# Kernel optimization log

Hardware: AMD Instinct MI355X
Metric: run time of the kernel (lower is better)

The kernel has to match this reference:

```python
import jax, jax.numpy as jnp
import numpy as np

DIM = 1024
NUM_HEADS = 16
HEAD_DIM = DIM // NUM_HEADS


def setup_inputs() -> dict:
    key = jax.random.key(0)
    k1, k2, k3, k4, k5 = jax.random.split(key, 5)
    B, N, C = 8, 1024, DIM
    x = jax.random.normal(k1, (B, N, C), dtype=jnp.float32)
    s_in = 1.0 / np.sqrt(C)
    w_qkv = jax.random.normal(k2, (C, 3 * C), dtype=jnp.float32) * s_in
    b_qkv = jnp.zeros((3 * C,), dtype=jnp.float32)
    w_proj = jax.random.normal(k3, (C, C), dtype=jnp.float32) * s_in
    b_proj = jnp.zeros((C,), dtype=jnp.float32)
    return {"x": x, "w_qkv": w_qkv, "b_qkv": b_qkv, "w_proj": w_proj, "b_proj": b_proj}


def reference(x, w_qkv, b_qkv, w_proj, b_proj):
    B, N, C = x.shape
    H, D = NUM_HEADS, C // NUM_HEADS
    scale = jnp.float32(1.0) / jnp.sqrt(jnp.float32(D))
    qkv = x @ w_qkv + b_qkv                      # [B, N, 3C]
    qkv = qkv.reshape(B, N, 3, H, D)
    qkv = jnp.transpose(qkv, (2, 0, 3, 1, 4))     # [3, B, H, N, D]
    q, k, v = qkv[0], qkv[1], qkv[2]
    attn = jnp.einsum('bhnd,bhmd->bhnm', q, k) * scale  # [B, H, N, N]
    attn = jax.nn.softmax(attn, axis=-1)
    out = jnp.einsum('bhnm,bhmd->bhnd', attn, v)  # [B, H, N, D]
    out = jnp.transpose(out, (0, 2, 1, 3)).reshape(B, N, C)
    return out @ w_proj + b_proj
```

## Files before the change

### kernel.cpp

```cpp
#include <hip/hip_runtime.h>
#include <stdint.h>
#include <stddef.h>


#define DEVI __device__ __forceinline__

typedef float f32x4 __attribute__((ext_vector_type(4)));
typedef float f32x16 __attribute__((ext_vector_type(16)));
typedef __bf16 bf16x8 __attribute__((ext_vector_type(8)));
typedef unsigned short u16x8 __attribute__((ext_vector_type(8)));
typedef unsigned short u16x4 __attribute__((ext_vector_type(4)));
typedef unsigned int u32;
typedef unsigned int u32x4 __attribute__((ext_vector_type(4)));

static constexpr int M1 = 8192;

DEVI unsigned short f2bf(float f) {
  uint32_t u = __builtin_bit_cast(uint32_t, f);
  u += 0x7FFFu + ((u >> 16) & 1u);
  return (unsigned short)(u >> 16);
}

DEVI float fexp2(float x) {
  float r;
  asm("v_exp_f32 %0, %1" : "=v"(r) : "v"(x));
  return r;
}

DEVI u32 cvtpk(float lo, float hi) {
  u32 r;
  asm("v_cvt_pk_bf16_f32 %0, %1, %2" : "=v"(r) : "v"(lo), "v"(hi));
  return r;
}

DEVI void plswap(u32& a, u32& b) {
  asm("v_permlane32_swap_b32 %0, %1" : "+v"(a), "+v"(b));
}

DEVI void gll16(const unsigned short* g, unsigned short* lds) {
  __builtin_amdgcn_global_load_lds(
      (const __attribute__((address_space(1))) void*)g,
      (__attribute__((address_space(3))) void*)lds, 16, 0, 0);
}

DEVI bf16x8 lds_frag(const unsigned short* p) {
  return __builtin_bit_cast(bf16x8, *(const u16x8*)p);
}

__global__ void k_cvt(const float* __restrict__ in, unsigned short* __restrict__ out, int n4) {
  int i = blockIdx.x * blockDim.x + threadIdx.x;
  if (i < n4) {
    float4 v = reinterpret_cast<const float4*>(in)[i];
    u16x4 o = { f2bf(v.x), f2bf(v.y), f2bf(v.z), f2bf(v.w) };
    reinterpret_cast<u16x4*>(out)[i] = o;
  }
}

__global__ void k_tr_cvt(const float* __restrict__ in, unsigned short* __restrict__ out,
                         int R, int Cc) {
  __shared__ float tile[32][33];
  int c0 = blockIdx.x * 32, r0 = blockIdx.y * 32;
  int tx = threadIdx.x, ty = threadIdx.y;
#pragma unroll
  for (int j = 0; j < 32; j += 8)
    tile[ty + j][tx] = in[(size_t)(r0 + ty + j) * Cc + c0 + tx];
  __syncthreads();
#pragma unroll
  for (int j = 0; j < 32; j += 8)
    out[(size_t)(c0 + ty + j) * R + r0 + tx] = f2bf(tile[tx][ty + j]);
}

__global__ void k_tr_v(const unsigned short* __restrict__ in, unsigned short* __restrict__ out) {
  __shared__ unsigned short t[32][33];
  int d0 = blockIdx.x * 32, n0 = blockIdx.y * 32, bh = blockIdx.z;
  const unsigned short* ip = in + (size_t)bh * 1024 * 64;
  unsigned short* op = out + (size_t)bh * 64 * 1024;
  int tx = threadIdx.x, ty = threadIdx.y;
#pragma unroll
  for (int j = 0; j < 32; j += 8)
    t[ty + j][tx] = ip[(size_t)(n0 + ty + j) * 64 + d0 + tx];
  __syncthreads();
#pragma unroll
  for (int j = 0; j < 32; j += 8)
    op[(size_t)(d0 + ty + j) * 1024 + n0 + tx] = t[tx][ty + j];
}

template <int EPI, int NCOLS>
__global__ __launch_bounds__(256, 2)
void k_gemm(const unsigned short* __restrict__ A,
            const unsigned short* __restrict__ Bt,
            const float* __restrict__ bias,
            unsigned short* __restrict__ Qp,
            unsigned short* __restrict__ Kp,
            unsigned short* __restrict__ Vp,
            float* __restrict__ Out) {
  constexpr int K = 1024, NK = K / 32;
  __shared__ unsigned short As[2][128 * 32];
  __shared__ unsigned short Bs[2][128 * 32];

  const int tid = threadIdx.x;
  const int w = tid >> 6, l = tid & 63;
  const int ln = l & 15, kg = l >> 4;
  const int wr = w >> 1, wc = w & 1;

  const int rt = blockIdx.x % (M1 / 128);
  const int ct = blockIdx.x / (M1 / 128);
  const int row0 = rt * 128, col0 = ct * 128;

  f32x4 acc[4][4] = {};

  const unsigned short* Ag = A + (size_t)row0 * K;
  const unsigned short* Bg = Bt + (size_t)col0 * K;

  auto stage = [&](int buf, int kt) {
    const unsigned short* ga = Ag + kt * 32;
    const unsigned short* gb = Bg + kt * 32;
#pragma unroll
    for (int j = 0; j < 2; j++) {
      int c = j * 256 + w * 64 + l;
      int r = c >> 2, s = c & 3;
      int ss = s ^ ((r >> 1) & 3);
      gll16(ga + (size_t)r * K + ss * 8, &As[buf][(j * 256 + w * 64) * 8]);
      gll16(gb + (size_t)r * K + ss * 8, &Bs[buf][(j * 256 + w * 64) * 8]);
    }
  };

  stage(0, 0);
  __syncthreads();

  int buf = 0;
  for (int kt = 0; kt < NK; kt++) {
    if (kt + 1 < NK) stage(buf ^ 1, kt + 1);

    bf16x8 af[4], bfr[4];
#pragma unroll
    for (int m = 0; m < 4; m++) {
      int r = wr * 64 + m * 16 + ln;
      int sl = kg ^ ((r >> 1) & 3);
      af[m] = lds_frag(&As[buf][r * 32 + sl * 8]);
    }
#pragma unroll
    for (int n = 0; n < 4; n++) {
      int r = wc * 64 + n * 16 + ln;
      int sl = kg ^ ((r >> 1) & 3);
      bfr[n] = lds_frag(&Bs[buf][r * 32 + sl * 8]);
    }
    __builtin_amdgcn_s_setprio(1);
#pragma unroll
    for (int m = 0; m < 4; m++)
#pragma unroll
      for (int n = 0; n < 4; n++)
        acc[m][n] = __builtin_amdgcn_mfma_f32_16x16x32_bf16(af[m], bfr[n], acc[m][n], 0, 0, 0);
    __builtin_amdgcn_s_setprio(0);

    __syncthreads();
    buf ^= 1;
  }

  constexpr float QS = 0.18033688011112042f;
  float bv[4];
#pragma unroll
  for (int n = 0; n < 4; n++) bv[n] = bias[col0 + wc * 64 + n * 16 + ln];

  if constexpr (EPI == 1) {
    const int three = col0 >> 10;
    const int h = ((col0 & 1023) >> 6) + wc;
    unsigned short* tgt = (three == 0) ? Qp : (three == 1) ? Kp : Vp;
    const float sc = (three == 0) ? QS : 1.f;
#pragma unroll
    for (int m = 0; m < 4; m++)
#pragma unroll
      for (int r = 0; r < 4; r++) {
        int row = row0 + wr * 64 + m * 16 + kg * 4 + r;
        int bb = row >> 10, nn = row & 1023;
        size_t base = ((size_t)(bb * 16 + h) * 1024 + nn) * 64;
#pragma unroll
        for (int n = 0; n < 4; n++)
          tgt[base + n * 16 + ln] = f2bf((acc[m][n][r] + bv[n]) * sc);
      }
  } else {
#pragma unroll
    for (int m = 0; m < 4; m++)
#pragma unroll
      for (int r = 0; r < 4; r++) {
        int row = row0 + wr * 64 + m * 16 + kg * 4 + r;
#pragma unroll
        for (int n = 0; n < 4; n++)
          Out[(size_t)row * 1024 + col0 + wc * 64 + n * 16 + ln] = acc[m][n][r] + bv[n];
      }
  }
}

__global__ __launch_bounds__(256, 4)
void k_attn(const unsigned short* __restrict__ Qg, const unsigned short* __restrict__ Kg,
            const unsigned short* __restrict__ Vtg, unsigned short* __restrict__ AO) {
  __shared__ unsigned short Ks[2][64 * 64];
  __shared__ unsigned short Vs[2][64 * 64];

  const int tid = threadIdx.x;
  const int w = tid >> 6, l = tid & 63;
  const int lq = l & 31, b = l >> 5;

  const int bh = blockIdx.x;
  const int qt = blockIdx.y;
  const int qbase = qt * 128 + w * 32;

  bf16x8 qf[4];
#pragma unroll
  for (int kk = 0; kk < 4; kk++) {
    size_t off = ((size_t)bh * 1024 + qbase + lq) * 64 + kk * 16 + b * 8;
    qf[kk] = __builtin_bit_cast(bf16x8, *(const u16x8*)(Qg + off));
  }

  f32x16 acc[2] = {};
  float mrun = -1e30f, lrun = 0.f;

  const unsigned short* Kbh = Kg + (size_t)bh * 1024 * 64;
  const unsigned short* Vbh = Vtg + (size_t)bh * 64 * 1024;

  auto stage = [&](int buf, int t) {
#pragma unroll
    for (int j = 0; j < 2; j++) {
      int c = j * 256 + w * 64 + l;
      int r = c >> 3, s = c & 7;
      int ss = s ^ (r & 7);
      gll16(Kbh + (size_t)(t * 64 + r) * 64 + ss * 8, &Ks[buf][(j * 256 + w * 64) * 8]);
      gll16(Vbh + (size_t)r * 1024 + t * 64 + ss * 8, &Vs[buf][(j * 256 + w * 64) * 8]);
    }
  };

  stage(0, 0);
  __syncthreads();

  int buf = 0;
  for (int t = 0; t < 16; t++) {
    if (t + 1 < 16) stage(buf ^ 1, t + 1);

    f32x16 s[2];
    __builtin_amdgcn_s_setprio(1);
#pragma unroll
    for (int kb = 0; kb < 2; kb++) {
      f32x16 z = {};
#pragma unroll
      for (int kk = 0; kk < 4; kk++) {
        int row = kb * 32 + lq;
        int ss = (kk * 2 + b) ^ (row & 7);
        bf16x8 kf = lds_frag(&Ks[buf][row * 64 + ss * 8]);
        z = __builtin_amdgcn_mfma_f32_32x32x16_bf16(kf, qf[kk], z, 0, 0, 0);
      }
      s[kb] = z;
    }
    __builtin_amdgcn_s_setprio(0);

    float tm = s[0][0];
#pragma unroll
    for (int kb = 0; kb < 2; kb++)
#pragma unroll
      for (int r = 0; r < 16; r++) tm = fmaxf(tm, s[kb][r]);
    tm = fmaxf(tm, __shfl_xor(tm, 32));

    if (!__all(tm <= mrun + 8.f)) {
      float mnew = fmaxf(mrun, tm);
      float al = fexp2(mrun - mnew);
      mrun = mnew;
      lrun *= al;
#pragma unroll
      for (int r = 0; r < 16; r++) {
        float aq = __shfl(al, (r & 3) + 8 * (r >> 2) + 4 * b);
        acc[0][r] *= aq;
        acc[1][r] *= aq;
      }
    }

    float rs = 0.f;
#pragma unroll
    for (int kb = 0; kb < 2; kb++)
#pragma unroll
      for (int r = 0; r < 16; r++) {
        float pv = fexp2(s[kb][r] - mrun);
        s[kb][r] = pv;
        rs += pv;
      }
    rs += __shfl_xor(rs, 32);
    lrun += rs;

    bf16x8 pa[4];
#pragma unroll
    for (int kb = 0; kb < 2; kb++) {
      u32 pk[4][2];
#pragma unroll
      for (int t4 = 0; t4 < 4; t4++) {
        pk[t4][0] = cvtpk(s[kb][t4 * 4 + 0], s[kb][t4 * 4 + 1]);
        pk[t4][1] = cvtpk(s[kb][t4 * 4 + 2], s[kb][t4 * 4 + 3]);
      }
#pragma unroll
      for (int sh = 0; sh < 2; sh++) {
        u32 a0 = pk[2 * sh][0], b0 = pk[2 * sh + 1][0];
        plswap(a0, b0);
        u32 a1 = pk[2 * sh][1], b1 = pk[2 * sh + 1][1];
        plswap(a1, b1);
        u32x4 fr = { a0, a1, b0, b1 };
        pa[kb * 2 + sh] = __builtin_bit_cast(bf16x8, fr);
      }
    }

    __builtin_amdgcn_s_setprio(1);
#pragma unroll
    for (int n = 0; n < 2; n++) {
#pragma unroll
      for (int st = 0; st < 4; st++) {
        int row = n * 32 + lq;
        int ss = (st * 2 + b) ^ (row & 7);
        bf16x8 vb = lds_frag(&Vs[buf][row * 64 + ss * 8]);
        acc[n] = __builtin_amdgcn_mfma_f32_32x32x16_bf16(pa[st], vb, acc[n], 0, 0, 0);
      }
    }
    __builtin_amdgcn_s_setprio(0);

    __syncthreads();
    buf ^= 1;
  }

  const int bb = bh >> 4, h = bh & 15;
  float linv = 1.f / lrun;
#pragma unroll
  for (int r = 0; r < 16; r++) {
    float lq_r = __shfl(linv, (r & 3) + 8 * (r >> 2) + 4 * b);
    int row = qbase + (r & 3) + 8 * (r >> 2) + 4 * b;
    size_t base = ((size_t)(bb * 1024 + row)) * 1024 + h * 64;
#pragma unroll
    for (int n = 0; n < 2; n++)
      AO[base + n * 32 + lq] = f2bf(acc[n][r] * lq_r);
  }
}

extern "C" void kernel_launch(void* const* d_in, const int* in_sizes, int n_in,
                              void* d_out, int out_size, void* d_ws, size_t ws_size,
                              hipStream_t stream) {
  const float* x      = (const float*)d_in[0];
  const float* w_qkv  = (const float*)d_in[1];
  const float* b_qkv  = (const float*)d_in[2];
  const float* w_proj = (const float*)d_in[3];
  const float* b_proj = (const float*)d_in[4];
  float* out = (float*)d_out;

  constexpr size_t SZ_XB  = (size_t)8192 * 1024 * 2;
  constexpr size_t SZ_WQ  = (size_t)3072 * 1024 * 2;
  constexpr size_t SZ_WP  = (size_t)1024 * 1024 * 2;
  constexpr size_t SZ_QKV = (size_t)8 * 16 * 1024 * 64 * 2;
  char* ws = (char*)d_ws;
  unsigned short* xb     = (unsigned short*)(ws);
  unsigned short* wqkvT  = (unsigned short*)(ws + SZ_XB);
  unsigned short* wprojT = (unsigned short*)(ws + SZ_XB + SZ_WQ);
  unsigned short* Qb     = (unsigned short*)(ws + SZ_XB + SZ_WQ + SZ_WP);
  unsigned short* Kb     = (unsigned short*)(ws + SZ_XB + SZ_WQ + SZ_WP + SZ_QKV);
  unsigned short* Vtb    = (unsigned short*)(ws + SZ_XB + SZ_WQ + SZ_WP + 2 * SZ_QKV);
  unsigned short* VrawAO = (unsigned short*)(ws + SZ_XB + SZ_WQ + SZ_WP + 3 * SZ_QKV);
  size_t needed = SZ_XB + SZ_WQ + SZ_WP + 4 * SZ_QKV;
  if (ws_size < needed) return;

  k_cvt<<<8192, 256, 0, stream>>>(x, xb, 8192 * 1024 / 4);
  dim3 tb(32, 8);
  k_tr_cvt<<<dim3(96, 32), tb, 0, stream>>>(w_qkv, wqkvT, 1024, 3072);
  k_tr_cvt<<<dim3(32, 32), tb, 0, stream>>>(w_proj, wprojT, 1024, 1024);
  k_gemm<1, 3072><<<64 * 24, 256, 0, stream>>>(xb, wqkvT, b_qkv, Qb, Kb, VrawAO, nullptr);
  k_tr_v<<<dim3(2, 32, 128), tb, 0, stream>>>(VrawAO, Vtb);
  k_attn<<<dim3(128, 8), 256, 0, stream>>>(Qb, Kb, Vtb, VrawAO);
  k_gemm<2, 1024><<<64 * 8, 256, 0, stream>>>(VrawAO, wprojT, b_proj, nullptr, nullptr, nullptr, out);
}
```

Measured before the change: 246.2 us.

## Replace QKV GEMM with 256x256-tile, 8-wave pipelined kernel

Adds a dedicated QKV projection kernel that uses 256x256 output tiles with K=64 steps, 512 threads, and XOR-swizzled LDS layout. Global loads are staggered into phased quarter-tile MFMA sub-steps with explicit barriers and vmcnt waits, and a block-index swizzle is added for L2 locality. Larger tiles raise arithmetic intensity and reduce global traffic, but each block uses more LDS and registers, and the hand-tuned wait counts must match the issue order exactly. The generic GEMM is trimmed to the output-projection epilogue only.

```diff
diff --git a/kernel.cpp b/kernel.cpp
--- a/kernel.cpp
+++ b/kernel.cpp
@@ -85,14 +85,178 @@
     op[(size_t)(d0 + ty + j) * 1024 + n0 + tx] = t[tx][ty + j];
 }
 
+__global__ __launch_bounds__(512, 2)
+void k_gemm1(const unsigned short* __restrict__ A,
+             const unsigned short* __restrict__ Bt,
+             const float* __restrict__ bias,
+             unsigned short* __restrict__ Qp,
+             unsigned short* __restrict__ Kp,
+             unsigned short* __restrict__ Vp) {
+  constexpr int K = 1024, NT = K / 64;
+  __shared__ unsigned short As[2 * 256 * 64];
+  __shared__ unsigned short Bs[2 * 256 * 64];
+
+  const int tid = threadIdx.x;
+  const int w = tid >> 6, l = tid & 63;
+  const int ln = l & 15, kg = l >> 4;
+  const int wr = w >> 2, wc = w & 3;
+
+  const int bid = blockIdx.x;
+  const int swz = (bid & 7) * 48 + (bid >> 3);
+  const int rt = swz & 31, ct = swz >> 5;
+  const int row0 = rt * 256, col0 = ct * 256;
+
+  const unsigned short* Ag = A + (size_t)row0 * K;
+  const unsigned short* Bg = Bt + (size_t)col0 * K;
+
+  auto stageA = [&](int kt, int hf) {
+    unsigned short* lb = &As[((kt & 1) * 256 + hf * 128) * 64];
+#pragma unroll
+    for (int j = 0; j < 2; j++) {
+      int idx = j * 512 + tid;
+      int r = idx >> 3, c = idx & 7;
+      gll16(Ag + (size_t)(hf * 128 + r) * K + kt * 64 + ((c ^ (r & 7)) * 8), lb + idx * 8);
+    }
+  };
+  auto stageB = [&](int kt, int hf) {
+    unsigned short* lb = &Bs[((kt & 1) * 256 + hf * 128) * 64];
+#pragma unroll
+    for (int j = 0; j < 2; j++) {
+      int idx = j * 512 + tid;
+      int r = idx >> 3, c = idx & 7;
+      gll16(Bg + (size_t)(hf * 128 + r) * K + kt * 64 + ((c ^ (r & 7)) * 8), lb + idx * 8);
+    }
+  };
+
+  f32x4 acc[8][4] = {};
+  bf16x8 am[4][2], b0[2][2], b1[2][2];
+
+  stageA(0, 0); stageA(0, 1); stageB(0, 0); stageB(0, 1);
+  stageA(1, 0); stageB(1, 0); stageB(1, 1);
+  asm volatile("s_waitcnt vmcnt(6)" ::: "memory");
+  __builtin_amdgcn_s_barrier();
+
+  for (int T = 0; T < NT; T++) {
+    const int dbase = (T & 1) * 256 * 64;
+
+#pragma unroll
+    for (int mi = 0; mi < 4; mi++)
+#pragma unroll
+      for (int kk = 0; kk < 2; kk++) {
+        int r = wr * 128 + mi * 16 + ln;
+        int c = (kk * 4 + kg) ^ (r & 7);
+        am[mi][kk] = lds_frag(&As[dbase + r * 64 + c * 8]);
+      }
+#pragma unroll
+    for (int ni = 0; ni < 2; ni++)
+#pragma unroll
+      for (int kk = 0; kk < 2; kk++) {
+        int r = wc * 64 + ni * 16 + ln;
+        int c = (kk * 4 + kg) ^ (r & 7);
+        b0[ni][kk] = lds_frag(&Bs[dbase + r * 64 + c * 8]);
+      }
+    if (T + 1 < NT) stageA(T + 1, 1);
+    __builtin_amdgcn_s_barrier();
+    asm volatile("s_waitcnt lgkmcnt(0)" ::: "memory");
+    __builtin_amdgcn_sched_barrier(0);
+    __builtin_amdgcn_s_setprio(1);
+#pragma unroll
+    for (int mi = 0; mi < 4; mi++)
+#pragma unroll
+      for (int ni = 0; ni < 2; ni++)
+#pragma unroll
+        for (int kk = 0; kk < 2; kk++)
+          acc[mi][ni] = __builtin_amdgcn_mfma_f32_16x16x32_bf16(am[mi][kk], b0[ni][kk], acc[mi][ni], 0, 0, 0);
+    __builtin_amdgcn_s_setprio(0);
+    __builtin_amdgcn_s_barrier();
+
+#pragma unroll
+    for (int ni = 0; ni < 2; ni++)
+#pragma unroll
+      for (int kk = 0; kk < 2; kk++) {
+        int r = wc * 64 + (2 + ni) * 16 + ln;
+        int c = (kk * 4 + kg) ^ (r & 7);
+        b1[ni][kk] = lds_frag(&Bs[dbase + r * 64 + c * 8]);
+      }
+    __builtin_amdgcn_s_barrier();
+    asm volatile("s_waitcnt lgkmcnt(0)" ::: "memory");
+    __builtin_amdgcn_sched_barrier(0);
+    __builtin_amdgcn_s_setprio(1);
+#pragma unroll
+    for (int mi = 0; mi < 4; mi++)
+#pragma unroll
+      for (int ni = 0; ni < 2; ni++)
+#pragma unroll
+        for (int kk = 0; kk < 2; kk++)
+          acc[mi][2 + ni] = __builtin_amdgcn_mfma_f32_16x16x32_bf16(am[mi][kk], b1[ni][kk], acc[mi][2 + ni], 0, 0, 0);
+    __builtin_amdgcn_s_setprio(0);
+    __builtin_amdgcn_s_barrier();
+
+#pragma unroll
+    for (int mi = 0; mi < 4; mi++)
+#pragma unroll
+      for (int kk = 0; kk < 2; kk++) {
+        int r = wr * 128 + (4 + mi) * 16 + ln;
+        int c = (kk * 4 + kg) ^ (r & 7);
+        am[mi][kk] = lds_frag(&As[dbase + r * 64 + c * 8]);
+      }
+    if (T + 2 < NT) stageB(T + 2, 0);
+    __builtin_amdgcn_s_barrier();
+    asm volatile("s_waitcnt lgkmcnt(0)" ::: "memory");
+    __builtin_amdgcn_sched_barrier(0);
+    __builtin_amdgcn_s_setprio(1);
+#pragma unroll
+    for (int mi = 0; mi < 4; mi++)
+#pragma unroll
+      for (int ni = 0; ni < 2; ni++)
+#pragma unroll
+        for (int kk = 0; kk < 2; kk++)
+          acc[4 + mi][2 + ni] = __builtin_amdgcn_mfma_f32_16x16x32_bf16(am[mi][kk], b1[ni][kk], acc[4 + mi][2 + ni], 0, 0, 0);
+    __builtin_amdgcn_s_setprio(0);
+    __builtin_amdgcn_s_barrier();
+
+    if (T + 2 < NT) { stageB(T + 2, 1); stageA(T + 2, 0); }
+    __builtin_amdgcn_s_barrier();
+    __builtin_amdgcn_s_setprio(1);
+#pragma unroll
+    for (int mi = 0; mi < 4; mi++)
+#pragma unroll
+      for (int ni = 0; ni < 2; ni++)
+#pragma unroll
+        for (int kk = 0; kk < 2; kk++)
+          acc[4 + mi][ni] = __builtin_amdgcn_mfma_f32_16x16x32_bf16(am[mi][kk], b0[ni][kk], acc[4 + mi][ni], 0, 0, 0);
+    __builtin_amdgcn_s_setprio(0);
+    if (T + 2 < NT)      asm volatile("s_waitcnt vmcnt(6)" ::: "memory");
+    else if (T + 1 < NT) asm volatile("s_waitcnt vmcnt(0)" ::: "memory");
+    __builtin_amdgcn_s_barrier();
+  }
+
+  constexpr float QS = 0.18033688011112042f;
+  const int three = col0 >> 10;
+  const int hh = ((col0 & 1023) >> 6) + wc;
+  unsigned short* tgt = (three == 0) ? Qp : (three == 1) ? Kp : Vp;
+  const float sc = (three == 0) ? QS : 1.f;
+  float bv[4];
+#pragma unroll
+  for (int n = 0; n < 4; n++) bv[n] = bias[col0 + wc * 64 + n * 16 + ln];
+#pragma unroll
+  for (int m = 0; m < 8; m++)
+#pragma unroll
+    for (int r = 0; r < 4; r++) {
+      int row = row0 + wr * 128 + m * 16 + kg * 4 + r;
+      int bb = row >> 10, nn = row & 1023;
+      size_t base = ((size_t)(bb * 16 + hh) * 1024 + nn) * 64;
+#pragma unroll
+      for (int n = 0; n < 4; n++)
+        tgt[base + n * 16 + ln] = f2bf((acc[m][n][r] + bv[n]) * sc);
+    }
+}
+
 template <int EPI, int NCOLS>
 __global__ __launch_bounds__(256, 2)
 void k_gemm(const unsigned short* __restrict__ A,
             const unsigned short* __restrict__ Bt,
             const float* __restrict__ bias,
-            unsigned short* __restrict__ Qp,
-            unsigned short* __restrict__ Kp,
-            unsigned short* __restrict__ Vp,
             float* __restrict__ Out) {
   constexpr int K = 1024, NK = K / 32;
   __shared__ unsigned short As[2][128 * 32];
@@ -157,38 +321,18 @@
     buf ^= 1;
   }
 
-  constexpr float QS = 0.18033688011112042f;
   float bv[4];
 #pragma unroll
   for (int n = 0; n < 4; n++) bv[n] = bias[col0 + wc * 64 + n * 16 + ln];
-
-  if constexpr (EPI == 1) {
-    const int three = col0 >> 10;
-    const int h = ((col0 & 1023) >> 6) + wc;
-    unsigned short* tgt = (three == 0) ? Qp : (three == 1) ? Kp : Vp;
-    const float sc = (three == 0) ? QS : 1.f;
-#pragma unroll
-    for (int m = 0; m < 4; m++)
-#pragma unroll
-      for (int r = 0; r < 4; r++) {
-        int row = row0 + wr * 64 + m * 16 + kg * 4 + r;
-        int bb = row >> 10, nn = row & 1023;
-        size_t base = ((size_t)(bb * 16 + h) * 1024 + nn) * 64;
-#pragma unroll
-        for (int n = 0; n < 4; n++)
-          tgt[base + n * 16 + ln] = f2bf((acc[m][n][r] + bv[n]) * sc);
-      }
-  } else {
-#pragma unroll
-    for (int m = 0; m < 4; m++)
-#pragma unroll
-      for (int r = 0; r < 4; r++) {
-        int row = row0 + wr * 64 + m * 16 + kg * 4 + r;
-#pragma unroll
-        for (int n = 0; n < 4; n++)
-          Out[(size_t)row * 1024 + col0 + wc * 64 + n * 16 + ln] = acc[m][n][r] + bv[n];
-      }
-  }
+#pragma unroll
+  for (int m = 0; m < 4; m++)
+#pragma unroll
+    for (int r = 0; r < 4; r++) {
+      int row = row0 + wr * 64 + m * 16 + kg * 4 + r;
+#pragma unroll
+      for (int n = 0; n < 4; n++)
+        Out[(size_t)row * 1024 + col0 + wc * 64 + n * 16 + ln] = acc[m][n][r] + bv[n];
+    }
 }
 
 __global__ __launch_bounds__(256, 4)
@@ -363,8 +507,8 @@
   dim3 tb(32, 8);
   k_tr_cvt<<<dim3(96, 32), tb, 0, stream>>>(w_qkv, wqkvT, 1024, 3072);
   k_tr_cvt<<<dim3(32, 32), tb, 0, stream>>>(w_proj, wprojT, 1024, 1024);
-  k_gemm<1, 3072><<<64 * 24, 256, 0, stream>>>(xb, wqkvT, b_qkv, Qb, Kb, VrawAO, nullptr);
+  k_gemm1<<<384, 512, 0, stream>>>(xb, wqkvT, b_qkv, Qb, Kb, VrawAO);
   k_tr_v<<<dim3(2, 32, 128), tb, 0, stream>>>(VrawAO, Vtb);
   k_attn<<<dim3(128, 8), 256, 0, stream>>>(Qb, Kb, Vtb, VrawAO);
-  k_gemm<2, 1024><<<64 * 8, 256, 0, stream>>>(VrawAO, wprojT, b_proj, nullptr, nullptr, nullptr, out);
-}
+  k_gemm<2, 1024><<<64 * 8, 256, 0, stream>>>(VrawAO, wprojT, b_proj, out);
+}
```

After: 250.2 us. About the same (+1.6%).
